# Kernel optimization log

Measured on AMD Instinct MI355X. Metric: run time of the kernel, lower is better.

## Reference

```python
import jax, jax.numpy as jnp
import numpy as np

NEG_FILL = -1e20
SPANS_PER_WORD = 2


def setup_inputs() -> dict:
    key = jax.random.key(0)
    k1, k2, k3, k4, k5 = jax.random.split(key, 5)
    B, N, D, T = 8, 16384, 256, 8
    embeddings = jax.random.normal(k1, (B, N, D), dtype=jnp.float32)
    scores_a = jax.random.normal(k2, (B, N, T), dtype=jnp.float32)
    scores_b = jax.random.normal(k3, (B, N, T), dtype=jnp.float32)
    span_mask = jax.random.randint(k4, (B, N), 0, 2).astype(bool)
    seq_length = jax.random.randint(k5, (B,), 1, 2048).astype(jnp.int32)
    return {
        "embeddings": embeddings,
        "scores_a": scores_a,
        "scores_b": scores_b,
        "span_mask": span_mask,
        "seq_length": seq_length,
    }


def reference(embeddings, scores_a, scores_b, span_mask, seq_length):
    # --- SpanPruner.forward: per-dict-entry softmax, drop null tag, max over tags ---
    probs_list = [jnp.max(jax.nn.softmax(s, axis=2)[:, :, 1:], axis=2)
                  for s in (scores_a, scores_b)]
    probabilities = jnp.maximum(probs_list[0], probs_list[1])  # max over dict entries  [B,N]

    # --- span_pruner ---
    num_keep = jnp.maximum(seq_length * SPANS_PER_WORD, 1)       # [B]
    max_keep = int(jnp.max(num_keep))                            # static k for topk

    scores = jnp.where(span_mask, probabilities, NEG_FILL)       # masked_fill  [B,N]
    _, top_indices = jax.lax.top_k(scores, max_keep)             # [B,K], descending like torch.topk

    top_indices_mask = jnp.arange(max_keep)[None, :] < num_keep[:, None]  # [B,K]
    fill_value = jnp.max(top_indices, axis=1, keepdims=True)
    top_indices = jnp.where(top_indices_mask, top_indices, fill_value)
    top_indices = jnp.sort(top_indices, axis=1)                  # [B,K]

    # batched_index_select gathers
    seq_mask = jnp.take_along_axis(span_mask, top_indices, axis=1)        # [B,K] bool
    top_mask = (top_indices_mask & seq_mask).astype(jnp.int32)            # [B,K]
    top_scores = jnp.take_along_axis(scores, top_indices, axis=1)         # [B,K]
    top_embeddings = jnp.take_along_axis(embeddings, top_indices[:, :, None], axis=1)  # [B,K,D]

    return top_indices, top_embeddings, top_scores, top_mask
```

## Files before the change

kernel.cpp:

```cpp
#include <hip/hip_runtime.h>
#include <math.h>

#define NB 8
#define NN 16384
#define NT 8
#define ND 256
#define NEG_FILL_F (-1e20f)

__device__ __forceinline__ unsigned fkey(float s){
  unsigned u = __float_as_uint(s);
  return (u & 0x80000000u) ? ~u : (u | 0x80000000u);
}
__device__ __forceinline__ float fkey_inv(unsigned k){
  unsigned u = (k & 0x80000000u) ? (k ^ 0x80000000u) : ~k;
  return __uint_as_float(u);
}

__device__ __forceinline__ float prob_of(const float4 x, const float4 y){
  float m = fmaxf(fmaxf(fmaxf(x.x,x.y),fmaxf(x.z,x.w)),
                  fmaxf(fmaxf(y.x,y.y),fmaxf(y.z,y.w)));
  float e0=expf(x.x-m), e1=expf(x.y-m), e2=expf(x.z-m), e3=expf(x.w-m);
  float e4=expf(y.x-m), e5=expf(y.y-m), e6=expf(y.z-m), e7=expf(y.w-m);
  float sum = ((((((e0+e1)+e2)+e3)+e4)+e5)+e6)+e7;
  float pm = fmaxf(fmaxf(fmaxf(e1,e2),fmaxf(e3,e4)),fmaxf(fmaxf(e5,e6),e7));
  return pm/sum;
}

__global__ void k_scores(const float* __restrict__ sa, const float* __restrict__ sb,
                         const int* __restrict__ mask, unsigned* __restrict__ outk,
                         int* __restrict__ gpart){
  __shared__ int lh[256];
  const int t = threadIdx.x;
  lh[t] = 0;
  __syncthreads();
  int i = blockIdx.x*256 + t;
  const float4* pa = (const float4*)(sa + (size_t)i*NT);
  const float4* pb = (const float4*)(sb + (size_t)i*NT);
  float4 a0=pa[0], a1=pa[1], b0=pb[0], b1=pb[1];
  float p = fmaxf(prob_of(a0,a1), prob_of(b0,b1));
  unsigned k = fkey(mask[i] ? p : NEG_FILL_F);
  outk[i] = k;
  atomicAdd(&lh[k>>24], 1);
  __syncthreads();
  gpart[blockIdx.x*256 + t] = lh[t];
}

__device__ int block_scan_excl(int v, int* lds, int tid){
  __syncthreads();
  int lane = tid & 63, wave = tid >> 6;
  int x = v;
  #pragma unroll
  for (int off=1; off<64; off<<=1){
    int y = __shfl_up(x, off, 64);
    if (lane >= off) x += y;
  }
  if (lane == 63) lds[wave] = x;
  __syncthreads();
  if (wave == 0){
    int w = (lane < 16) ? lds[lane] : 0;
    #pragma unroll
    for (int off=1; off<16; off<<=1){
      int y = __shfl_up(w, off, 64);
      if (lane >= off) w += y;
    }
    if (lane < 16) lds[16+lane] = w;
  }
  __syncthreads();
  int waveOff = wave ? lds[16+wave-1] : 0;
  return waveOff + x - v;
}

__device__ void scan_pick2(int x, int r0, int r1, bool do1,
                           int* P, int* lds4, int* sOut, int tid, int lane, int wave){
  int Pt = 0;
  if (tid < 256){
    #pragma unroll
    for (int off=1; off<64; off<<=1){
      int y = __shfl_up(x, off, 64);
      if (lane >= off) x += y;
    }
    if (lane==63) lds4[wave] = x;
    Pt = x;
  }
  __syncthreads();
  if (tid < 256){
    int offs = 0;
    for (int w=0; w<wave; ++w) offs += lds4[w];
    Pt += offs;
    P[tid] = Pt;
  }
  __syncthreads();
  if (tid < 256){
    int prev = tid ? P[tid-1] : 0;
    if (Pt >= r0 && prev < r0){ sOut[0] = 255-tid; sOut[1] = r0-prev; }
    if (do1 && Pt >= r1 && prev < r1){ sOut[2] = 255-tid; sOut[3] = r1-prev; }
  }
  __syncthreads();
}

__global__ __launch_bounds__(1024)
void k_select(const unsigned* __restrict__ keys, const int* __restrict__ gpart,
              const int* __restrict__ seq, float* __restrict__ out, int K){
  const int b = blockIdx.x;
  const int tid = threadIdx.x;
  const int lane = tid & 63, wave = tid >> 6;
  __shared__ unsigned whA[16][257];
  __shared__ unsigned whB[16][257];
  __shared__ int part4[4][256];
  __shared__ int histA[256];
  __shared__ int histB[256];
  __shared__ int P[256];
  __shared__ int lds[32];
  __shared__ int lds4[4];
  __shared__ int smax[16];
  __shared__ int sOut[8];
  __shared__ int sFill;

  int num_keep = seq[b]*2; if (num_keep < 1) num_keep = 1;

  {
    int grp = tid >> 8;
    int bin = tid & 255;
    const int* gp = gpart + (b*64 + grp*16)*256 + bin;
    int sum = 0;
    #pragma unroll
    for (int w=0; w<16; ++w) sum += gp[w*256];
    part4[grp][bin] = sum;
  }

  const unsigned* kb = keys + (size_t)b*NN + tid*16;
  unsigned kk[16];
  #pragma unroll
  for (int q=0;q<4;++q){
    uint4 v = ((const uint4*)kb)[q];
    kk[4*q+0]=v.x; kk[4*q+1]=v.y; kk[4*q+2]=v.z; kk[4*q+3]=v.w;
  }
  __syncthreads();

  int r0 = K, r1 = num_keep;
  int x0 = 0;
  if (tid < 256){
    int bin = 255 - tid;
    x0 = part4[0][bin] + part4[1][bin] + part4[2][bin] + part4[3][bin];
  }
  scan_pick2(x0, r0, r1, true, P, lds4, sOut, tid, lane, wave);
  unsigned pref0 = (unsigned)sOut[0] << 24;  r0 = sOut[1];
  unsigned pref1 = (unsigned)sOut[2] << 24;  r1 = sOut[3];
  bool same = (pref0 == pref1);
  unsigned decided = 0xFF000000u;
  __syncthreads();

  for (int round=1; round<4; ++round){
    const int shift = 24 - 8*round;
    #pragma unroll
    for (int i=0;i<4;++i){
      whA[wave][lane + 64*i] = 0u;
      whB[wave][lane + 64*i] = 0u;
    }
    __syncthreads();
    const bool dual = !same;
    #pragma unroll
    for (int j=0;j<16;++j){
      unsigned k = kk[j];
      if (((k ^ pref0) & decided) == 0u)
        atomicAdd(&whA[wave][(k>>shift)&255u], 1u);
      if (dual && ((k ^ pref1) & decided) == 0u)
        atomicAdd(&whB[wave][(k>>shift)&255u], 1u);
    }
    __syncthreads();
    if (tid < 256){
      unsigned sa_=0, sb_=0;
      #pragma unroll
      for (int w=0;w<16;++w){ sa_ += whA[w][tid]; sb_ += whB[w][tid]; }
      histA[tid] = (int)sa_;
      histB[tid] = (int)sb_;
    }
    __syncthreads();
    int xa = (tid < 256) ? histA[255-tid] : 0;
    scan_pick2(xa, r0, r1, same, P, lds4, sOut, tid, lane, wave);
    if (dual){
      int xb = (tid < 256) ? histB[255-tid] : 0;
      scan_pick2(xb, r1, 0, false, P, lds4, sOut+4, tid, lane, wave);
    }
    int bin0 = sOut[0], rem0 = sOut[1];
    int bin1 = dual ? sOut[4] : sOut[2];
    int rem1 = dual ? sOut[5] : sOut[3];
    __syncthreads();
    pref0 |= (unsigned)bin0 << shift;  r0 = rem0;
    pref1 |= (unsigned)bin1 << shift;  r1 = rem1;
    same = same && (bin0 == bin1);
    decided |= (0xFFu << shift);
  }
  const unsigned TK = pref0;  const int needK = r0;
  const unsigned TN = pref1;  const int needN = r1;

  int cTK=0, cTN=0;
  #pragma unroll
  for (int j=0;j<16;++j){
    unsigned k = kk[j];
    cTK += (k==TK); cTN += (k==TN);
  }
  int packed = block_scan_excl((cTK<<16)|cTN, lds, tid);
  int oTK = (packed>>16)&0xFFFF, oTN = packed&0xFFFF;

  const int base = tid*16;
  int tK=oTK, tN=oTN, cKept=0, maxIdx=-1;
  #pragma unroll
  for (int j=0;j<16;++j){
    unsigned k=kk[j];
    bool inK  = (k>TK) || ((k==TK) && (tK<needK));  if (k==TK) tK++;
    bool kept = (k>TN) || ((k==TN) && (tN<needN));  if (k==TN) tN++;
    if (inK) maxIdx = base+j;
    cKept += kept;
  }
  int oKept = block_scan_excl(cKept, lds, tid);

  int mv=maxIdx;
  #pragma unroll
  for (int off=32; off; off>>=1){
    int y = __shfl_down(mv, off, 64);
    mv = mv > y ? mv : y;
  }
  if (lane==0) smax[wave]=mv;
  __syncthreads();
  if (tid==0){
    int f=-1;
    #pragma unroll
    for (int i=0;i<16;++i) f = f > smax[i] ? f : smax[i];
    sFill = f;
  }
  __syncthreads();
  const int fill = sFill;

  float* out_idx = out;
  float* out_sc  = out + (size_t)NB*K + (size_t)NB*K*ND;
  float* out_mk  = out_sc + (size_t)NB*K;
  const int ob = b*K;
  const unsigned kNEG = fkey(NEG_FILL_F);

  int tN2=oTN, p=oKept;
  #pragma unroll
  for (int j=0;j<16;++j){
    unsigned k=kk[j];
    bool kept = (k>TN) || ((k==TN) && (tN2<needN));  if (k==TN) tN2++;
    if (kept){
      int n = base+j;
      out_idx[ob+p] = (float)n;
      out_sc[ob+p]  = fkey_inv(k);
      out_mk[ob+p]  = (k != kNEG) ? 1.0f : 0.0f;
      ++p;
    }
  }
  if (num_keep < K){
    float fs = fkey_inv(keys[(size_t)b*NN + fill]);
    for (int q = num_keep + tid; q < K; q += 1024){
      out_idx[ob+q] = (float)fill;
      out_sc[ob+q]  = fs;
      out_mk[ob+q]  = 0.0f;
    }
  }
}

__global__ void k_gather(const float* __restrict__ emb, const float* __restrict__ out_idx,
                         float* __restrict__ out_emb, int K){
  int b = blockIdx.y;
  int g = blockIdx.x*256 + threadIdx.x;
  if (g >= K*64) return;
  int c = g & 63;
  int p = g >> 6;
  size_t r = (size_t)b*K + p;
  int idx = (int)out_idx[r];
  const float4* src = (const float4*)(emb + ((size_t)b*NN + (size_t)idx)*ND);
  float4* dst = (float4*)(out_emb + r*(size_t)ND);
  dst[c] = src[c];
}

extern "C" void kernel_launch(void* const* d_in, const int* in_sizes, int n_in,
                              void* d_out, int out_size, void* d_ws, size_t ws_size,
                              hipStream_t stream) {
  const float* emb  = (const float*)d_in[0];
  const float* sa   = (const float*)d_in[1];
  const float* sb   = (const float*)d_in[2];
  const int*   mask = (const int*)d_in[3];
  const int*   seq  = (const int*)d_in[4];
  float* out = (float*)d_out;
  unsigned* ws_keys = (unsigned*)d_ws;
  int* gpart = (int*)d_ws + (size_t)NB*NN;

  int K = out_size / (NB*(ND+3));
  if (K <= 0) return;

  k_scores<<<(NB*NN)/256, 256, 0, stream>>>(sa, sb, mask, ws_keys, gpart);
  k_select<<<NB, 1024, 0, stream>>>(ws_keys, gpart, seq, out, K);
  dim3 ggrid((K*64 + 255)/256, NB);
  k_gather<<<ggrid, 256, 0, stream>>>(emb, out, out + (size_t)NB*K, K);
}
```

Before: 205.7 us.

## Use two 12-bit radix rounds with shared 4096-bin histograms in top-k select

The radix select now runs two 12-bit refinement rounds on a single shared 4096-bin histogram per target, replacing three 8-bit rounds on per-wave privatized histograms that needed a reduction step. Threshold-bin picking uses a block-wide scan over four bins per thread. The kept-count prefix is now derived from one packed 64-bit scan of equal and greater counts, removing a second block scan. This cuts rounds and barriers but adds atomic contention on the shared histogram and more LDS to clear and scan.

```diff
diff --git a/kernel.cpp b/kernel.cpp
--- a/kernel.cpp
+++ b/kernel.cpp
@@ -70,30 +70,46 @@
   return waveOff + x - v;
 }
 
-__device__ void scan_pick2(int x, int r0, int r1, bool do1,
-                           int* P, int* lds4, int* sOut, int tid, int lane, int wave){
-  int Pt = 0;
-  if (tid < 256){
-    #pragma unroll
-    for (int off=1; off<64; off<<=1){
-      int y = __shfl_up(x, off, 64);
-      if (lane >= off) x += y;
-    }
-    if (lane==63) lds4[wave] = x;
-    Pt = x;
-  }
-  __syncthreads();
-  if (tid < 256){
-    int offs = 0;
-    for (int w=0; w<wave; ++w) offs += lds4[w];
-    Pt += offs;
-    P[tid] = Pt;
-  }
-  __syncthreads();
-  if (tid < 256){
-    int prev = tid ? P[tid-1] : 0;
-    if (Pt >= r0 && prev < r0){ sOut[0] = 255-tid; sOut[1] = r0-prev; }
-    if (do1 && Pt >= r1 && prev < r1){ sOut[2] = 255-tid; sOut[3] = r1-prev; }
+__device__ unsigned long long block_scan_excl_u64(unsigned long long v,
+                                                  unsigned long long* lds, int tid){
+  __syncthreads();
+  int lane = tid & 63, wave = tid >> 6;
+  unsigned long long x = v;
+  #pragma unroll
+  for (int off=1; off<64; off<<=1){
+    unsigned long long y = __shfl_up(x, off, 64);
+    if (lane >= off) x += y;
+  }
+  if (lane == 63) lds[wave] = x;
+  __syncthreads();
+  if (wave == 0){
+    unsigned long long w = (lane < 16) ? lds[lane] : 0ull;
+    #pragma unroll
+    for (int off=1; off<16; off<<=1){
+      unsigned long long y = __shfl_up(w, off, 64);
+      if (lane >= off) w += y;
+    }
+    if (lane < 16) lds[16+lane] = w;
+  }
+  __syncthreads();
+  unsigned long long waveOff = wave ? lds[16+wave-1] : 0ull;
+  return waveOff + x - v;
+}
+
+__device__ void scan_pick4k(const int* __restrict__ hist, int r0, int r1, bool do1,
+                            int* lds, int* sOut, int tid){
+  int s[4];
+  const int d0 = tid*4;
+  #pragma unroll
+  for (int i=0;i<4;++i) s[i] = hist[4095 - (d0+i)];
+  int tot = s[0]+s[1]+s[2]+s[3];
+  int c = block_scan_excl(tot, lds, tid);
+  #pragma unroll
+  for (int i=0;i<4;++i){
+    int nc = c + s[i];
+    if (c < r0 && nc >= r0){ sOut[0] = 4095-(d0+i); sOut[1] = r0 - c; }
+    if (do1 && c < r1 && nc >= r1){ sOut[2] = 4095-(d0+i); sOut[3] = r1 - c; }
+    c = nc;
   }
   __syncthreads();
 }
@@ -104,14 +120,11 @@
   const int b = blockIdx.x;
   const int tid = threadIdx.x;
   const int lane = tid & 63, wave = tid >> 6;
-  __shared__ unsigned whA[16][257];
-  __shared__ unsigned whB[16][257];
   __shared__ int part4[4][256];
-  __shared__ int histA[256];
-  __shared__ int histB[256];
-  __shared__ int P[256];
+  __shared__ int histA[4096];
+  __shared__ int histB[4096];
   __shared__ int lds[32];
-  __shared__ int lds4[4];
+  __shared__ unsigned long long ldsL[32];
   __shared__ int smax[16];
   __shared__ int sOut[8];
   __shared__ int sFill;
@@ -143,19 +156,29 @@
     int bin = 255 - tid;
     x0 = part4[0][bin] + part4[1][bin] + part4[2][bin] + part4[3][bin];
   }
-  scan_pick2(x0, r0, r1, true, P, lds4, sOut, tid, lane, wave);
-  unsigned pref0 = (unsigned)sOut[0] << 24;  r0 = sOut[1];
-  unsigned pref1 = (unsigned)sOut[2] << 24;  r1 = sOut[3];
+  {
+    int pre = block_scan_excl(x0, lds, tid);
+    if (tid < 256){
+      int nc = pre + x0;
+      if (pre < r0 && nc >= r0){ sOut[0] = 255-tid; sOut[1] = r0-pre; }
+      if (pre < r1 && nc >= r1){ sOut[2] = 255-tid; sOut[3] = r1-pre; }
+    }
+    __syncthreads();
+  }
+  unsigned pref0 = (unsigned)sOut[0] << 24;  int r0n = sOut[1];
+  unsigned pref1 = (unsigned)sOut[2] << 24;  int r1n = sOut[3];
+  r0 = r0n; r1 = r1n;
   bool same = (pref0 == pref1);
   unsigned decided = 0xFF000000u;
   __syncthreads();
 
-  for (int round=1; round<4; ++round){
-    const int shift = 24 - 8*round;
+  #pragma unroll
+  for (int round=0; round<2; ++round){
+    const int shift = 12 - 12*round;
     #pragma unroll
     for (int i=0;i<4;++i){
-      whA[wave][lane + 64*i] = 0u;
-      whB[wave][lane + 64*i] = 0u;
+      histA[tid + 1024*i] = 0;
+      histB[tid + 1024*i] = 0;
     }
     __syncthreads();
     const bool dual = !same;
@@ -163,25 +186,13 @@
     for (int j=0;j<16;++j){
       unsigned k = kk[j];
       if (((k ^ pref0) & decided) == 0u)
-        atomicAdd(&whA[wave][(k>>shift)&255u], 1u);
+        atomicAdd(&histA[(k>>shift)&0xFFFu], 1);
       if (dual && ((k ^ pref1) & decided) == 0u)
-        atomicAdd(&whB[wave][(k>>shift)&255u], 1u);
+        atomicAdd(&histB[(k>>shift)&0xFFFu], 1);
     }
     __syncthreads();
-    if (tid < 256){
-      unsigned sa_=0, sb_=0;
-      #pragma unroll
-      for (int w=0;w<16;++w){ sa_ += whA[w][tid]; sb_ += whB[w][tid]; }
-      histA[tid] = (int)sa_;
-      histB[tid] = (int)sb_;
-    }
-    __syncthreads();
-    int xa = (tid < 256) ? histA[255-tid] : 0;
-    scan_pick2(xa, r0, r1, same, P, lds4, sOut, tid, lane, wave);
-    if (dual){
-      int xb = (tid < 256) ? histB[255-tid] : 0;
-      scan_pick2(xb, r1, 0, false, P, lds4, sOut+4, tid, lane, wave);
-    }
+    scan_pick4k(histA, r0, r1, same, lds, sOut, tid);
+    if (dual) scan_pick4k(histB, r1, 0, false, lds, sOut+4, tid);
     int bin0 = sOut[0], rem0 = sOut[1];
     int bin1 = dual ? sOut[4] : sOut[2];
     int rem1 = dual ? sOut[5] : sOut[3];
@@ -189,32 +200,33 @@
     pref0 |= (unsigned)bin0 << shift;  r0 = rem0;
     pref1 |= (unsigned)bin1 << shift;  r1 = rem1;
     same = same && (bin0 == bin1);
-    decided |= (0xFFu << shift);
+    decided |= (0xFFFu << shift);
   }
   const unsigned TK = pref0;  const int needK = r0;
   const unsigned TN = pref1;  const int needN = r1;
 
-  int cTK=0, cTN=0;
+  int cTK=0, cTN=0, cGT=0;
   #pragma unroll
   for (int j=0;j<16;++j){
     unsigned k = kk[j];
-    cTK += (k==TK); cTN += (k==TN);
-  }
-  int packed = block_scan_excl((cTK<<16)|cTN, lds, tid);
-  int oTK = (packed>>16)&0xFFFF, oTN = packed&0xFFFF;
+    cTK += (k==TK); cTN += (k==TN); cGT += (k>TN);
+  }
+  unsigned long long pk = block_scan_excl_u64(
+      ((unsigned long long)cTK<<42) | ((unsigned long long)cTN<<21) | (unsigned long long)cGT,
+      ldsL, tid);
+  const int oTK = (int)(pk>>42);
+  const int oTN = (int)((pk>>21) & 0x1FFFFFu);
+  const int oGT = (int)(pk & 0x1FFFFFu);
+  const int oKept = oGT + min(needN, oTN);
 
   const int base = tid*16;
-  int tK=oTK, tN=oTN, cKept=0, maxIdx=-1;
+  int tK=oTK, maxIdx=-1;
   #pragma unroll
   for (int j=0;j<16;++j){
     unsigned k=kk[j];
-    bool inK  = (k>TK) || ((k==TK) && (tK<needK));  if (k==TK) tK++;
-    bool kept = (k>TN) || ((k==TN) && (tN<needN));  if (k==TN) tN++;
+    bool inK = (k>TK) || ((k==TK) && (tK<needK));  if (k==TK) tK++;
     if (inK) maxIdx = base+j;
-    cKept += kept;
-  }
-  int oKept = block_scan_excl(cKept, lds, tid);
-
+  }
   int mv=maxIdx;
   #pragma unroll
   for (int off=32; off; off>>=1){
```

After: 203.1 us. Within noise of the previous version (-1.3%).
